# Performance work log

Measured on AMD Instinct MI355X. Metric: run time of the kernel, lower is better.

Reference implementation:

```python
import jax, jax.numpy as jnp
import numpy as np

NF, NLOC, NNEI = 4, 2048, 64
EMBED, PAIR_DIM, H = 128, 64, 8
HD = EMBED // H
EPS = 1e-5

def _ln(x, g, b):
    m = x.mean(-1, keepdims=True)
    v = ((x - m) ** 2).mean(-1, keepdims=True)
    return (x - m) * jax.lax.rsqrt(v + EPS) * g + b

def setup_inputs() -> dict:
    key = jax.random.key(0)
    ks = jax.random.split(key, 12)
    inp = {
        "query": jax.random.normal(ks[0], (NF, NLOC, EMBED), jnp.float32),
        "pair": jax.random.normal(ks[1], (NF, NLOC, NNEI, PAIR_DIM), jnp.float32),
        "nlist": jax.random.randint(ks[2], (NF, NLOC, NNEI), 0, NLOC, jnp.int64),
        "delta_pos": jax.random.normal(ks[3], (NF, NLOC, NNEI, 3), jnp.float32),
        "attn_mask": jnp.zeros((NF, H, NLOC, NNEI), jnp.float32),
        "ln_g": jnp.ones((EMBED,), jnp.float32),
        "ln_b": jnp.zeros((EMBED,), jnp.float32),
        "pn_g": jnp.ones((PAIR_DIM,), jnp.float32),
        "pn_b": jnp.zeros((PAIR_DIM,), jnp.float32),
        "Wq": jax.random.normal(ks[4], (EMBED, EMBED), jnp.float32) * (EMBED ** -0.5),
        "Wk": jax.random.normal(ks[5], (EMBED, EMBED), jnp.float32) * (EMBED ** -0.5),
        "Wv": jax.random.normal(ks[6], (EMBED, EMBED), jnp.float32) * (EMBED ** -0.5),
        "Wbias": jax.random.normal(ks[7], (H, PAIR_DIM), jnp.float32) * (PAIR_DIM ** -0.5),
        "bbias": jnp.zeros((H,), jnp.float32),
        "Wforce": jax.random.normal(ks[8], (1, EMBED), jnp.float32) * (EMBED ** -0.5),
    }
    return inp

def reference(query, pair, nlist, delta_pos, attn_mask,
              ln_g, ln_b, pn_g, pn_b, Wq, Wk, Wv, Wbias, bbias, Wforce):
    nf, nloc, _ = query.shape
    nnei = nlist.shape[-1]
    qn = _ln(query, ln_g, ln_b)            # [f,l,e]
    pn = _ln(pair, pn_g, pn_b)             # [f,l,n,p]
    scaling = HD ** -0.5
    q = (qn @ Wq.T).reshape(nf, nloc, H, HD) * scaling       # [f,l,h,d]
    k = qn @ Wk.T                                            # [f,l,e]
    v = qn @ Wv.T
    idx = nlist.reshape(nf, -1)[..., None]                   # [f,l*n,1]
    kg = jnp.take_along_axis(k, idx, axis=1).reshape(nf, nloc, nnei, H, HD)
    vg = jnp.take_along_axis(v, idx, axis=1).reshape(nf, nloc, nnei, H, HD)
    attn = jnp.einsum('flhd,flnhd->fhln', q, kg)             # [f,h,l,n]
    bias = jnp.einsum('flnp,hp->fhln', pn, Wbias) + bbias[None, :, None, None]
    probs = jax.nn.softmax(attn + attn_mask + bias, axis=-1)  # dropout off (eval)
    # rotate by delta_pos and contract with v over neighbors
    x = jnp.einsum('fhln,flnc,flnhd->flchd', probs, delta_pos, vg)
    x = x.reshape(nf, nloc, 3, EMBED)
    force = (x @ Wforce.T).squeeze(-1)                       # [f,l,3]
    return force
```

## Files before the change

### kernel.cpp

```cpp
#include <hip/hip_runtime.h>

#define NFR   4
#define NLOCC 2048
#define NNEIN 64
#define EMB   128
#define PDIM  64
#define NH    8
#define LNEPS 1e-5f
#define NROW  (NFR*NLOCC)

#define WS_Q   0
#define WS_K   (NROW*EMB)
#define WS_FV  (2*NROW*EMB)
#define WS_G   (2*NROW*EMB + NROW*NH)

__device__ __forceinline__ void fma4(float4& acc, const float4 a, const float4 b) {
    acc.x = fmaf(a.x, b.x, acc.x);
    acc.y = fmaf(a.y, b.y, acc.y);
    acc.z = fmaf(a.z, b.z, acc.z);
    acc.w = fmaf(a.w, b.w, acc.w);
}
__device__ __forceinline__ void fma4s(float4& acc, const float s, const float4 b) {
    acc.x = fmaf(s, b.x, acc.x);
    acc.y = fmaf(s, b.y, acc.y);
    acc.z = fmaf(s, b.z, acc.z);
    acc.w = fmaf(s, b.w, acc.w);
}
__device__ __forceinline__ float hsum4(const float4 a) {
    return (a.x + a.y) + (a.z + a.w);
}
__device__ __forceinline__ float dot4(const float4 a, const float4 b) {
    return fmaf(a.x, b.x, fmaf(a.y, b.y, fmaf(a.z, b.z, a.w * b.w)));
}
__device__ __forceinline__ float4 scale4(const float4 a, const float s) {
    return make_float4(a.x*s, a.y*s, a.z*s, a.w*s);
}

__global__ __launch_bounds__(256, 2) void qkfv_kernel(
    const float* __restrict__ query,
    const float* __restrict__ ln_g, const float* __restrict__ ln_b,
    const float* __restrict__ Wq, const float* __restrict__ Wk,
    const float* __restrict__ Wv, const float* __restrict__ Wforce,
    const float* __restrict__ pn_g, const float* __restrict__ pn_b,
    const float* __restrict__ Wbias, const float* __restrict__ bbias,
    float* __restrict__ ws)
{
    __shared__ float  gb_s[2][EMB];
    __shared__ float  qn_s[16*132];
    __shared__ float  wt_s[2][16*132];
    __shared__ float4 wvf_s4[8*33];
    const int t = threadIdx.x;
    const int rowbase = blockIdx.x * 16;

    if (t < 64) {
        const float* src = (t < 32) ? ln_g : ln_b;
        ((float4*)gb_s[t >> 5])[t & 31] = ((const float4*)src)[t & 31];
    }

    if (blockIdx.x == 0) {
        if (t < 128) {
            const float4 wb4 = ((const float4*)Wbias)[t];
            const float4 pg4 = ((const float4*)pn_g)[t & 15];
            ((float4*)(ws + WS_G))[t] =
                make_float4(wb4.x*pg4.x, wb4.y*pg4.y, wb4.z*pg4.z, wb4.w*pg4.w);
        } else if (t < 192) {
            const int h = (t - 128) >> 3, s8 = (t - 128) & 7;
            float sg = 0.f, cb = 0.f;
            #pragma unroll
            for (int k = 0; k < 8; ++k) {
                const int p = s8*8 + k;
                const float wb = Wbias[h*PDIM + p];
                sg = fmaf(pn_g[p], wb, sg);
                cb = fmaf(pn_b[p], wb, cb);
            }
            sg += __shfl_xor(sg, 1, 64); sg += __shfl_xor(sg, 2, 64); sg += __shfl_xor(sg, 4, 64);
            cb += __shfl_xor(cb, 1, 64); cb += __shfl_xor(cb, 2, 64); cb += __shfl_xor(cb, 4, 64);
            if (s8 == 0) {
                ws[WS_G + 512 + h] = sg;
                ws[WS_G + 520 + h] = cb + bbias[h];
            }
        }
    }

    {
        const int h = t >> 5, ch = t & 31;
        float4 acc = make_float4(0.f, 0.f, 0.f, 0.f);
        #pragma unroll
        for (int d = 0; d < 16; ++d) {
            const float wf = Wforce[h*16 + d];
            const float4 wv = ((const float4*)(Wv + (size_t)(h*16 + d)*EMB))[ch];
            fma4s(acc, wf, wv);
        }
        wvf_s4[h*33 + ch] = acc;
    }

    const int r   = t >> 4;
    const int seg = t & 15;
    float4 x0 = ((const float4*)query)[(size_t)(rowbase + r)*32 + seg*2 + 0];
    float4 x1 = ((const float4*)query)[(size_t)(rowbase + r)*32 + seg*2 + 1];
    float s  = (x0.x + x0.y) + (x0.z + x0.w) + (x1.x + x1.y) + (x1.z + x1.w);
    float ss = x0.x*x0.x + x0.y*x0.y + x0.z*x0.z + x0.w*x0.w
             + x1.x*x1.x + x1.y*x1.y + x1.z*x1.z + x1.w*x1.w;
    #pragma unroll
    for (int m = 1; m < 16; m <<= 1) {
        s  += __shfl_xor(s,  m, 64);
        ss += __shfl_xor(ss, m, 64);
    }
    const float mean = s * (1.0f / 128.0f);
    const float var  = ss * (1.0f / 128.0f) - mean * mean;
    const float rstd = rsqrtf(var + LNEPS);
    __syncthreads();

    {
        const int c0 = seg * 8;
        float4 o0, o1;
        o0.x = (x0.x - mean)*rstd*gb_s[0][c0+0] + gb_s[1][c0+0];
        o0.y = (x0.y - mean)*rstd*gb_s[0][c0+1] + gb_s[1][c0+1];
        o0.z = (x0.z - mean)*rstd*gb_s[0][c0+2] + gb_s[1][c0+2];
        o0.w = (x0.w - mean)*rstd*gb_s[0][c0+3] + gb_s[1][c0+3];
        o1.x = (x1.x - mean)*rstd*gb_s[0][c0+4] + gb_s[1][c0+4];
        o1.y = (x1.y - mean)*rstd*gb_s[0][c0+5] + gb_s[1][c0+5];
        o1.z = (x1.z - mean)*rstd*gb_s[0][c0+6] + gb_s[1][c0+6];
        o1.w = (x1.w - mean)*rstd*gb_s[0][c0+7] + gb_s[1][c0+7];
        ((float4*)qn_s)[r*33 + seg*2 + 0] = o0;
        ((float4*)qn_s)[r*33 + seg*2 + 1] = o1;
    }
    __syncthreads();

    const int rp = t >> 5;
    const int r0 = rp * 2;
    const int cq = t & 31;
    const int sc0 = t >> 2;
    const int si0 = t & 3;
    const float4* qn4 = (const float4*)qn_s;

    for (int w = 0; w < 2; ++w) {
        const float4* W4 = (const float4*)((w == 0) ? Wq : Wk);
        float4 acc0 = make_float4(0.f,0.f,0.f,0.f);
        float4 acc1 = make_float4(0.f,0.f,0.f,0.f);
        {
            float4 g0 = W4[(size_t)sc0*32 + si0];
            float4 g1 = W4[(size_t)(sc0+64)*32 + si0];
            float* wt = wt_s[0];
            wt[(si0*4+0)*132 + sc0] = g0.x; wt[(si0*4+1)*132 + sc0] = g0.y;
            wt[(si0*4+2)*132 + sc0] = g0.z; wt[(si0*4+3)*132 + sc0] = g0.w;
            wt[(si0*4+0)*132 + sc0+64] = g1.x; wt[(si0*4+1)*132 + sc0+64] = g1.y;
            wt[(si0*4+2)*132 + sc0+64] = g1.z; wt[(si0*4+3)*132 + sc0+64] = g1.w;
        }
        __syncthreads();
        #pragma unroll
        for (int tau = 0; tau < 8; ++tau) {
            const int buf = tau & 1;
            float4 ng0, ng1;
            if (tau < 7) {
                ng0 = W4[(size_t)sc0*32 + (tau+1)*4 + si0];
                ng1 = W4[(size_t)(sc0+64)*32 + (tau+1)*4 + si0];
            }
            const float4* wt4 = (const float4*)wt_s[buf];
            #pragma unroll
            for (int e4 = 0; e4 < 4; ++e4) {
                float4 a0 = qn4[r0*33 + tau*4 + e4];
                float4 a1 = qn4[(r0+1)*33 + tau*4 + e4];
                const float* a0p = (const float*)&a0;
                const float* a1p = (const float*)&a1;
                #pragma unroll
                for (int ee = 0; ee < 4; ++ee) {
                    const float4 wv = wt4[(e4*4+ee)*33 + cq];
                    fma4s(acc0, a0p[ee], wv);
                    fma4s(acc1, a1p[ee], wv);
                }
            }
            if (tau < 7) {
                float* wt = wt_s[buf ^ 1];
                wt[(si0*4+0)*132 + sc0] = ng0.x; wt[(si0*4+1)*132 + sc0] = ng0.y;
                wt[(si0*4+2)*132 + sc0] = ng0.z; wt[(si0*4+3)*132 + sc0] = ng0.w;
                wt[(si0*4+0)*132 + sc0+64] = ng1.x; wt[(si0*4+1)*132 + sc0+64] = ng1.y;
                wt[(si0*4+2)*132 + sc0+64] = ng1.z; wt[(si0*4+3)*132 + sc0+64] = ng1.w;
            }
            __syncthreads();
        }
        const float sc = (w == 0) ? 0.25f : 1.0f;
        float4* dst = (float4*)(ws + (w == 0 ? WS_Q : WS_K));
        dst[(size_t)(rowbase + r0)*32 + cq]     = scale4(acc0, sc);
        dst[(size_t)(rowbase + r0 + 1)*32 + cq] = scale4(acc1, sc);
    }

    if (t < 128) {
        const int rr = t >> 3, h = t & 7;
        float4 acc = make_float4(0.f,0.f,0.f,0.f);
        #pragma unroll
        for (int ch = 0; ch < 32; ++ch)
            fma4(acc, qn4[rr*33 + ch], wvf_s4[h*33 + ch]);
        ws[WS_FV + (size_t)(rowbase + rr)*NH + h] = hsum4(acc);
    }
}

__global__ __launch_bounds__(256, 8) void attn_force_kernel(
    const float* __restrict__ pair, const int* __restrict__ nlist,
    const float* __restrict__ delta_pos, const float* __restrict__ attn_mask,
    const float* __restrict__ ws, float* __restrict__ out)
{
    __shared__ float4 q_s4[4*32];

    const int t    = threadIdx.x;
    const int w    = t >> 6;
    const int lane = t & 63;
    const int bid  = ((blockIdx.x & 7) << 8) | (blockIdx.x >> 3);
    const int row  = (bid << 2) | w;
    const int fr   = row >> 11;
    const int l    = row & (NLOCC - 1);
    const int n    = lane;

    if (lane < 32)
        q_s4[(w << 5) | lane] = ((const float4*)(ws + WS_Q))[(size_t)row*32 + lane];

    const int jn = nlist[(size_t)row*NNEIN + n];

    const float* dpp = delta_pos + ((size_t)row*NNEIN + n)*3;
    const float dpx = dpp[0], dpy = dpp[1], dpz = dpp[2];

    const float4* pr4 = (const float4*)(pair + ((size_t)row*NNEIN + n)*PDIM);
    const float4* Gg  = (const float4*)(ws + WS_G);
    float d[NH];
    #pragma unroll
    for (int h = 0; h < NH; ++h) d[h] = 0.f;
    float s = 0.f, ss = 0.f;
    #pragma unroll 4
    for (int c4 = 0; c4 < 16; ++c4) {
        const float4 p4 = pr4[c4];
        s  += hsum4(p4);
        ss += dot4(p4, p4);
        #pragma unroll
        for (int h = 0; h < NH; ++h)
            d[h] += dot4(p4, Gg[h*16 + c4]);
    }
    const float mean = s * (1.0f / 64.0f);
    const float var  = ss * (1.0f / 64.0f) - mean * mean;
    const float rstd = rsqrtf(var + LNEPS);

    float qk[NH];
    #pragma unroll
    for (int h = 0; h < NH; ++h) qk[h] = 0.f;
    const float4* k4   = (const float4*)(ws + WS_K) + ((size_t)(fr << 11) + jn)*32;
    const float4* qrow = &q_s4[w << 5];
    #pragma unroll 4
    for (int c4 = 0; c4 < 32; ++c4)
        qk[c4 >> 2] += dot4(k4[c4], qrow[c4]);

    const float* SGp = ws + WS_G + 512;
    float lg[NH];
    #pragma unroll
    for (int h = 0; h < NH; ++h)
        lg[h] = qk[h] + rstd*(d[h] - mean*SGp[h]) + SGp[8 + h]
              + attn_mask[(((size_t)(fr*NH + h))*NLOCC + l)*NNEIN + n];

    const float4* fvp = (const float4*)(ws + WS_FV + ((size_t)(fr << 11) + jn)*NH);
    const float4 fa = fvp[0];
    const float4 fb = fvp[1];

    float p[NH];
    #pragma unroll
    for (int h = 0; h < NH; ++h) {
        float m = lg[h];
        #pragma unroll
        for (int mm = 1; mm < 64; mm <<= 1)
            m = fmaxf(m, __shfl_xor(m, mm, 64));
        const float e = __expf(lg[h] - m);
        float sum = e;
        #pragma unroll
        for (int mm = 1; mm < 64; mm <<= 1)
            sum += __shfl_xor(sum, mm, 64);
        p[h] = e * (1.0f / sum);
    }

    const float sn = p[0]*fa.x + p[1]*fa.y + p[2]*fa.z + p[3]*fa.w
                   + p[4]*fb.x + p[5]*fb.y + p[6]*fb.z + p[7]*fb.w;
    float f0 = sn*dpx, f1 = sn*dpy, f2 = sn*dpz;
    #pragma unroll
    for (int mm = 1; mm < 64; mm <<= 1) {
        f0 += __shfl_xor(f0, mm, 64);
        f1 += __shfl_xor(f1, mm, 64);
        f2 += __shfl_xor(f2, mm, 64);
    }
    if (lane < 3)
        out[(size_t)row*3 + lane] = (lane == 0) ? f0 : ((lane == 1) ? f1 : f2);
}

extern "C" void kernel_launch(void* const* d_in, const int* in_sizes, int n_in,
                              void* d_out, int out_size, void* d_ws, size_t ws_size,
                              hipStream_t stream) {
    const float* query     = (const float*)d_in[0];
    const float* pair      = (const float*)d_in[1];
    const int*   nlist     = (const int*)d_in[2];
    const float* delta_pos = (const float*)d_in[3];
    const float* attn_mask = (const float*)d_in[4];
    const float* ln_g      = (const float*)d_in[5];
    const float* ln_b      = (const float*)d_in[6];
    const float* pn_g      = (const float*)d_in[7];
    const float* pn_b      = (const float*)d_in[8];
    const float* Wq        = (const float*)d_in[9];
    const float* Wk        = (const float*)d_in[10];
    const float* Wv        = (const float*)d_in[11];
    const float* Wbias     = (const float*)d_in[12];
    const float* bbias     = (const float*)d_in[13];
    const float* Wforce    = (const float*)d_in[14];
    float* out = (float*)d_out;
    float* ws  = (float*)d_ws;

    qkfv_kernel<<<512, 256, 0, stream>>>(query, ln_g, ln_b, Wq, Wk, Wv, Wforce,
                                         pn_g, pn_b, Wbias, bbias, ws);
    attn_force_kernel<<<NROW/4, 256, 0, stream>>>(pair, nlist, delta_pos, attn_mask,
                                                  ws, out);
}
```

Before: 301.6 us.

## Restructure attention kernel: block per 4 rows, coalesced K gather, prefetch next row

Rewrites the attention/force kernel so each block handles four consecutive rows cooperatively. Threads split neighbors and channels so K rows are gathered as coalesced float4 loads, and the reductions use DPP intrinsics instead of full-wave shuffles. Logits, bias and fv go through shared memory, and softmax runs with one head per 32-lane group. Loads for the next row are software-pipelined in double-buffered registers, at the cost of more registers, lower occupancy (launch bounds 3) and two block barriers per row.

Measured after the change: 265.4 us. 12.0% less time.

```diff
diff --git a/kernel.cpp b/kernel.cpp
--- a/kernel.cpp
+++ b/kernel.cpp
@@ -34,6 +34,12 @@
 }
 __device__ __forceinline__ float4 scale4(const float4 a, const float s) {
     return make_float4(a.x*s, a.y*s, a.z*s, a.w*s);
+}
+
+template<int CTRL>
+__device__ __forceinline__ float dppf(float x) {
+    return __int_as_float(__builtin_amdgcn_update_dpp(
+        0, __float_as_int(x), CTRL, 0xF, 0xF, true));
 }
 
 __global__ __launch_bounds__(256, 2) void qkfv_kernel(
@@ -195,95 +201,172 @@
     }
 }
 
-__global__ __launch_bounds__(256, 8) void attn_force_kernel(
+
+#define ISSUE_INDEP(S, rrow)                                                        \
+    {                                                                               \
+        jnS[S] = nlist[(size_t)(rrow)*NNEIN + n];                                   \
+        q4S[S] = ((const float4*)(ws + WS_Q))[(size_t)(rrow)*32 + c];               \
+        const size_t mbase = (((size_t)(fr*NH + hh))*NLOCC + ((rrow) & (NLOCC-1)))*NNEIN; \
+        maS[S] = attn_mask[mbase + i32];                                            \
+        mbS[S] = attn_mask[mbase + i32 + 32];                                       \
+        const float4* prp = (const float4*)(pair + ((size_t)(rrow)*NNEIN + n)*PDIM) + sub*4; \
+        prS[S][0] = prp[0]; prS[S][1] = prp[1];                                     \
+        prS[S][2] = prp[2]; prS[S][3] = prp[3];                                     \
+        const float* dpp_ = delta_pos + (size_t)(rrow)*192;                         \
+        dpaS[S][0] = dpp_[i32*3+0]; dpaS[S][1] = dpp_[i32*3+1]; dpaS[S][2] = dpp_[i32*3+2]; \
+        dpbS[S][0] = dpp_[(i32+32)*3+0]; dpbS[S][1] = dpp_[(i32+32)*3+1]; dpbS[S][2] = dpp_[(i32+32)*3+2]; \
+    }
+
+#define ISSUE_GATHER(S, rrow)                                                       \
+    {                                                                               \
+        int j0 = nlist[(size_t)(rrow)*NNEIN + ((w << 4) | 0 | half)];               \
+        int j1 = nlist[(size_t)(rrow)*NNEIN + ((w << 4) | 2 | half)];               \
+        int j2 = nlist[(size_t)(rrow)*NNEIN + ((w << 4) | 4 | half)];               \
+        int j3 = nlist[(size_t)(rrow)*NNEIN + ((w << 4) | 6 | half)];               \
+        int j4 = nlist[(size_t)(rrow)*NNEIN + ((w << 4) | 8 | half)];               \
+        int j5 = nlist[(size_t)(rrow)*NNEIN + ((w << 4) | 10 | half)];              \
+        int j6 = nlist[(size_t)(rrow)*NNEIN + ((w << 4) | 12 | half)];              \
+        int j7 = nlist[(size_t)(rrow)*NNEIN + ((w << 4) | 14 | half)];              \
+        kk[0] = k4[(size_t)j0*32 + c]; kk[1] = k4[(size_t)j1*32 + c];               \
+        kk[2] = k4[(size_t)j2*32 + c]; kk[3] = k4[(size_t)j3*32 + c];               \
+        kk[4] = k4[(size_t)j4*32 + c]; kk[5] = k4[(size_t)j5*32 + c];               \
+        kk[6] = k4[(size_t)j6*32 + c]; kk[7] = k4[(size_t)j7*32 + c];               \
+        fvS[S] = ((const float2*)(fvb + (size_t)jnS[S]*NH))[sub];                   \
+    }
+
+#define ROW_BODY(CUR, NXT, rowc, PF)                                                \
+    {                                                                               \
+        fv_s[n*9 + sub*2]     = fvS[CUR].x;                                         \
+        fv_s[n*9 + sub*2 + 1] = fvS[CUR].y;                                         \
+        if (PF) ISSUE_INDEP(NXT, (rowc) + 1);                                       \
+                                          \
+        _Pragma("unroll")                                                           \
+        for (int i = 0; i < 8; ++i) {                                               \
+            float pp = dot4(kk[i], q4S[CUR]);                                       \
+            pp += dppf<0xB1>(pp);                                                   \
+            pp += dppf<0x4E>(pp);                                                   \
+            if ((c & 3) == 0)                                                       \
+                logit_s[((w << 4) | (i << 1) | half)*9 + (c >> 2)] = pp;            \
+        }                                                                           \
+        if (PF) ISSUE_GATHER(NXT, (rowc) + 1);                                      \
+                                             \
+        {                                                                           \
+            const float4 p0 = prS[CUR][0], p1 = prS[CUR][1];                        \
+            const float4 p2 = prS[CUR][2], p3 = prS[CUR][3];                        \
+            float s  = hsum4(p0) + hsum4(p1) + hsum4(p2) + hsum4(p3);               \
+            float ss = dot4(p0,p0) + dot4(p1,p1) + dot4(p2,p2) + dot4(p3,p3);       \
+            s  += dppf<0xB1>(s);  s  += dppf<0x4E>(s);                              \
+            ss += dppf<0xB1>(ss); ss += dppf<0x4E>(ss);                             \
+            float d[NH];                                                            \
+            _Pragma("unroll")                                                       \
+            for (int h = 0; h < NH; ++h) d[h] = 0.f;                                \
+            const float4* gw = &gw_s4[w << 7];                                      \
+            _Pragma("unroll")                                                       \
+            for (int h = 0; h < NH; ++h) {                                          \
+                d[h] += dot4(p0, gw[h*16 + sub*4 + 0]);                             \
+                d[h] += dot4(p1, gw[h*16 + sub*4 + 1]);                             \
+                d[h] += dot4(p2, gw[h*16 + sub*4 + 2]);                             \
+                d[h] += dot4(p3, gw[h*16 + sub*4 + 3]);                             \
+            }                                                                       \
+            _Pragma("unroll")                                                       \
+            for (int h = 0; h < NH; ++h) {                                          \
+                d[h] += dppf<0xB1>(d[h]);                                           \
+                d[h] += dppf<0x4E>(d[h]);                                           \
+            }                                                                       \
+            const float mean = s * (1.0f / 64.0f);                                  \
+            const float var  = ss * (1.0f / 64.0f) - mean * mean;                   \
+            const float rstd = rsqrtf(var + LNEPS);                                 \
+            const float* SGp = ws + WS_G + 512;                                     \
+            const int h0 = sub*2, h1 = h0 + 1;                                      \
+            bias_s[n*9 + h0] = rstd*(d[h0] - mean*SGp[h0]) + SGp[8 + h0];           \
+            bias_s[n*9 + h1] = rstd*(d[h1] - mean*SGp[h1]) + SGp[8 + h1];           \
+        }                                                                           \
+        __syncthreads();                       \
+                                         \
+        {                                                                           \
+            const float a = logit_s[i32*9 + hh]        + bias_s[i32*9 + hh]        + maS[CUR]; \
+            const float b = logit_s[(i32 + 32)*9 + hh] + bias_s[(i32 + 32)*9 + hh] + mbS[CUR]; \
+            float m = fmaxf(a, b);                                                  \
+            m = fmaxf(m, __shfl_xor(m, 16, 64));                                    \
+            m = fmaxf(m, __shfl_xor(m,  8, 64));                                    \
+            m = fmaxf(m, __shfl_xor(m,  4, 64));                                    \
+            m = fmaxf(m, dppf<0x4E>(m));                                            \
+            m = fmaxf(m, dppf<0xB1>(m));                                            \
+            const float ea = __expf(a - m), eb = __expf(b - m);                     \
+            float sum = ea + eb;                                                    \
+            sum += __shfl_xor(sum, 16, 64);                                         \
+            sum += __shfl_xor(sum,  8, 64);                                         \
+            sum += __shfl_xor(sum,  4, 64);                                         \
+            sum += dppf<0x4E>(sum);                                                 \
+            sum += dppf<0xB1>(sum);                                                 \
+            const float inv = 1.0f / sum;                                           \
+            const float ca = ea * inv * fv_s[i32*9 + hh];                           \
+            const float cb = eb * inv * fv_s[(i32 + 32)*9 + hh];                    \
+            float f0 = ca*dpaS[CUR][0] + cb*dpbS[CUR][0];                           \
+            float f1 = ca*dpaS[CUR][1] + cb*dpbS[CUR][1];                           \
+            float f2 = ca*dpaS[CUR][2] + cb*dpbS[CUR][2];                           \
+            f0 += dppf<0x111>(f0); f0 += dppf<0x112>(f0); f0 += dppf<0x114>(f0); f0 += dppf<0x118>(f0); \
+            f0 += dppf<0x142>(f0); f0 += dppf<0x143>(f0);                           \
+            f1 += dppf<0x111>(f1); f1 += dppf<0x112>(f1); f1 += dppf<0x114>(f1); f1 += dppf<0x118>(f1); \
+            f1 += dppf<0x142>(f1); f1 += dppf<0x143>(f1);                           \
+            f2 += dppf<0x111>(f2); f2 += dppf<0x112>(f2); f2 += dppf<0x114>(f2); f2 += dppf<0x118>(f2); \
+            f2 += dppf<0x142>(f2); f2 += dppf<0x143>(f2);                           \
+            if (lane == 63) {                                                       \
+                fpart[w][0] = f0; fpart[w][1] = f1; fpart[w][2] = f2;               \
+            }                                                                       \
+        }                                                                           \
+        __syncthreads();        \
+        if (t < 3)                                                                  \
+            out[(size_t)(rowc)*3 + t] = fpart[0][t] + fpart[1][t] + fpart[2][t] + fpart[3][t]; \
+    }
+
+__global__ __launch_bounds__(256, 3) void attn_force_kernel(
     const float* __restrict__ pair, const int* __restrict__ nlist,
     const float* __restrict__ delta_pos, const float* __restrict__ attn_mask,
     const float* __restrict__ ws, float* __restrict__ out)
 {
-    __shared__ float4 q_s4[4*32];
+    __shared__ float  logit_s[NNEIN*9];
+    __shared__ float  bias_s[NNEIN*9];
+    __shared__ float  fv_s[NNEIN*9];
+    __shared__ float4 gw_s4[4*128];
+    __shared__ float  fpart[4][3];
 
     const int t    = threadIdx.x;
+    const int row0 = blockIdx.x << 2;
+    const int fr   = row0 >> 11;
     const int w    = t >> 6;
     const int lane = t & 63;
-    const int bid  = ((blockIdx.x & 7) << 8) | (blockIdx.x >> 3);
-    const int row  = (bid << 2) | w;
-    const int fr   = row >> 11;
-    const int l    = row & (NLOCC - 1);
-    const int n    = lane;
-
-    if (lane < 32)
-        q_s4[(w << 5) | lane] = ((const float4*)(ws + WS_Q))[(size_t)row*32 + lane];
-
-    const int jn = nlist[(size_t)row*NNEIN + n];
-
-    const float* dpp = delta_pos + ((size_t)row*NNEIN + n)*3;
-    const float dpx = dpp[0], dpy = dpp[1], dpz = dpp[2];
-
-    const float4* pr4 = (const float4*)(pair + ((size_t)row*NNEIN + n)*PDIM);
-    const float4* Gg  = (const float4*)(ws + WS_G);
-    float d[NH];
-    #pragma unroll
-    for (int h = 0; h < NH; ++h) d[h] = 0.f;
-    float s = 0.f, ss = 0.f;
-    #pragma unroll 4
-    for (int c4 = 0; c4 < 16; ++c4) {
-        const float4 p4 = pr4[c4];
-        s  += hsum4(p4);
-        ss += dot4(p4, p4);
-        #pragma unroll
-        for (int h = 0; h < NH; ++h)
-            d[h] += dot4(p4, Gg[h*16 + c4]);
-    }
-    const float mean = s * (1.0f / 64.0f);
-    const float var  = ss * (1.0f / 64.0f) - mean * mean;
-    const float rstd = rsqrtf(var + LNEPS);
-
-    float qk[NH];
-    #pragma unroll
-    for (int h = 0; h < NH; ++h) qk[h] = 0.f;
-    const float4* k4   = (const float4*)(ws + WS_K) + ((size_t)(fr << 11) + jn)*32;
-    const float4* qrow = &q_s4[w << 5];
-    #pragma unroll 4
-    for (int c4 = 0; c4 < 32; ++c4)
-        qk[c4 >> 2] += dot4(k4[c4], qrow[c4]);
-
-    const float* SGp = ws + WS_G + 512;
-    float lg[NH];
-    #pragma unroll
-    for (int h = 0; h < NH; ++h)
-        lg[h] = qk[h] + rstd*(d[h] - mean*SGp[h]) + SGp[8 + h]
-              + attn_mask[(((size_t)(fr*NH + h))*NLOCC + l)*NNEIN + n];
-
-    const float4* fvp = (const float4*)(ws + WS_FV + ((size_t)(fr << 11) + jn)*NH);
-    const float4 fa = fvp[0];
-    const float4 fb = fvp[1];
-
-    float p[NH];
-    #pragma unroll
-    for (int h = 0; h < NH; ++h) {
-        float m = lg[h];
-        #pragma unroll
-        for (int mm = 1; mm < 64; mm <<= 1)
-            m = fmaxf(m, __shfl_xor(m, mm, 64));
-        const float e = __expf(lg[h] - m);
-        float sum = e;
-        #pragma unroll
-        for (int mm = 1; mm < 64; mm <<= 1)
-            sum += __shfl_xor(sum, mm, 64);
-        p[h] = e * (1.0f / sum);
-    }
-
-    const float sn = p[0]*fa.x + p[1]*fa.y + p[2]*fa.z + p[3]*fa.w
-                   + p[4]*fb.x + p[5]*fb.y + p[6]*fb.z + p[7]*fb.w;
-    float f0 = sn*dpx, f1 = sn*dpy, f2 = sn*dpz;
-    #pragma unroll
-    for (int mm = 1; mm < 64; mm <<= 1) {
-        f0 += __shfl_xor(f0, mm, 64);
-        f1 += __shfl_xor(f1, mm, 64);
-        f2 += __shfl_xor(f2, mm, 64);
-    }
-    if (lane < 3)
-        out[(size_t)row*3 + lane] = (lane == 0) ? f0 : ((lane == 1) ? f1 : f2);
+    const int n    = t >> 2;
+    const int sub  = t & 3;
+    const int half = lane >> 5;
+    const int c    = lane & 31;
+    const int hh   = t >> 5;
+    const int i32  = lane & 31;
+
+    {
+        const float4* Gg = (const float4*)(ws + WS_G);
+        gw_s4[(w << 7) | lane]        = Gg[lane];
+        gw_s4[(w << 7) | (64 + lane)] = Gg[64 + lane];
+    }
+
+    int    jnS[2];
+    float4 q4S[2];
+    float  maS[2], mbS[2];
+    float4 prS[2][4];
+    float  dpaS[2][3], dpbS[2][3];
+    float2 fvS[2];
+    float4 kk[8];
+
+    const float4* k4  = (const float4*)(ws + WS_K) + (size_t)(fr << 11)*32;
+    const float*  fvb = ws + WS_FV + ((size_t)(fr << 11))*NH;
+
+    ISSUE_INDEP(0, row0);
+    ISSUE_GATHER(0, row0);
+
+    ROW_BODY(0, 1, row0 + 0, 1);
+    ROW_BODY(1, 0, row0 + 1, 1);
+    ROW_BODY(0, 1, row0 + 2, 1);
+    ROW_BODY(1, 0, row0 + 3, 0);
 }
 
 extern "C" void kernel_launch(void* const* d_in, const int* in_sizes, int n_in,
```
